# Performance work log

Measured on AMD Instinct MI355X. Metric: run time of the kernel, lower is better.

## Reference

```python
import jax, jax.numpy as jnp
import numpy as np

N_NODES = 100000
N_EDGES = 1600000
HIDDEN = 128


def setup_inputs() -> dict:
    key = jax.random.key(0)
    k_x, k_w1, k_w2, k_v, k_i, k_o = jax.random.split(key, 6)
    x = jax.random.normal(k_x, (N_NODES, HIDDEN), dtype=jnp.float32)
    # gate1/gate2 are Linear(hidden,1,bias=False); store their weight rows as vectors
    w1 = jax.random.normal(k_w1, (HIDDEN,), dtype=jnp.float32) * 0.1
    w2 = jax.random.normal(k_w2, (HIDDEN,), dtype=jnp.float32) * 0.1
    adj_vals = jax.random.uniform(k_v, (N_EDGES,), dtype=jnp.float32)
    in_idx = jax.random.randint(k_i, (N_EDGES,), 0, N_NODES, dtype=jnp.int32)
    out_idx = jax.random.randint(k_o, (N_EDGES,), 0, N_NODES, dtype=jnp.int32)
    return {"x": x, "w1": w1, "w2": w2, "adj_vals": adj_vals,
            "in_idx": in_idx, "out_idx": out_idx}


def reference(x, w1, w2, adj_vals, in_idx, out_idx):
    # per-node gate scalars: x1 = gate1(x), x2 = gate2(x)  -> [N]
    x1 = x @ w1
    x2 = x @ w2
    # edge gate: tanh(x1[src] + x2[dst]) * adj_value  (dropout is identity in eval mode)
    m = jnp.tanh(x1[in_idx] + x2[out_idx]) * adj_vals  # [E]
    # sparse.mm(adj_alpha, x): out[i] = sum_{e: row(e)=i} m_e * x[col(e)]
    messages = m[:, None] * x[out_idx]                 # [E, d]
    result = jax.ops.segment_sum(messages, in_idx, num_segments=N_NODES)
    return result
```

## Files before the change

### kernel.cpp

```cpp
#include <hip/hip_runtime.h>

#define N_NODES 100000
#define N_EDGES 1600000
#define HIDDEN  128

#define NPB_SHIFT 9
#define NPB       512
#define NB        ((N_NODES + NPB - 1) / NPB)
#define PART_EPT  16
#define PART_EPB  (256 * PART_EPT)
#define PART_B    ((N_EDGES + PART_EPB - 1) / PART_EPB)

#define SCAN_C 16
#define SCAN_T ((N_NODES + SCAN_C - 1) / SCAN_C)
#define SCAN_THREADS 6400
#define SCAN_B (SCAN_THREADS / 256)

__device__ __forceinline__ ushort f2bf(float f) {
    unsigned int u = __float_as_uint(f);
    u = (u + 0x7FFFu + ((u >> 16) & 1u)) >> 16;
    return (ushort)u;
}

__global__ void fagcn_gates(const float* __restrict__ x,
                            const float* __restrict__ w1,
                            const float* __restrict__ w2,
                            float* __restrict__ g1,
                            float* __restrict__ g2,
                            int*   __restrict__ cursor,
                            int*   __restrict__ bcnt,
                            ushort* __restrict__ xh,
                            int write_xh) {
    const int tid  = blockIdx.x * blockDim.x + threadIdx.x;
    if (tid < NB) bcnt[tid] = 0;
    const int node = tid >> 5;
    const int hl   = (int)(threadIdx.x & 31);
    if (node >= N_NODES) return;

    const float4 xv  = *reinterpret_cast<const float4*>(x  + (size_t)node * HIDDEN + hl * 4);
    const float4 w1v = *reinterpret_cast<const float4*>(w1 + hl * 4);
    const float4 w2v = *reinterpret_cast<const float4*>(w2 + hl * 4);

    if (write_xh) {
        ushort4 h;
        h.x = f2bf(xv.x); h.y = f2bf(xv.y); h.z = f2bf(xv.z); h.w = f2bf(xv.w);
        *reinterpret_cast<ushort4*>(xh + (size_t)node * HIDDEN + hl * 4) = h;
    }

    float s1 = xv.x * w1v.x + xv.y * w1v.y + xv.z * w1v.z + xv.w * w1v.w;
    float s2 = xv.x * w2v.x + xv.y * w2v.y + xv.z * w2v.z + xv.w * w2v.w;

    #pragma unroll
    for (int off = 16; off > 0; off >>= 1) {
        s1 += __shfl_down(s1, off, 32);
        s2 += __shfl_down(s2, off, 32);
    }
    if (hl == 0) {
        g1[node] = s1;
        g2[node] = s2;
        cursor[node] = 0;
    }
}

__global__ void fagcn_histb(const int* __restrict__ in_idx,
                            int* __restrict__ bcnt) {
    __shared__ int cnt[NB];
    const int tid  = (int)threadIdx.x;
    const int base = blockIdx.x * PART_EPB + tid * PART_EPT;
    for (int j = tid; j < NB; j += 256) cnt[j] = 0;
    __syncthreads();
    if (base < N_EDGES) {
        #pragma unroll
        for (int i = 0; i < 4; ++i) {
            const int4 v = *reinterpret_cast<const int4*>(in_idx + base + i * 4);
            atomicAdd(&cnt[v.x >> NPB_SHIFT], 1);
            atomicAdd(&cnt[v.y >> NPB_SHIFT], 1);
            atomicAdd(&cnt[v.z >> NPB_SHIFT], 1);
            atomicAdd(&cnt[v.w >> NPB_SHIFT], 1);
        }
    }
    __syncthreads();
    for (int j = tid; j < NB; j += 256)
        if (cnt[j]) atomicAdd(&bcnt[j], cnt[j]);
}

__global__ void fagcn_scanb(const int* __restrict__ bcnt,
                            int* __restrict__ bbase,
                            int* __restrict__ bcur) {
    __shared__ int l[256];
    const int t = (int)threadIdx.x;
    const int c = (t < NB) ? bcnt[t] : 0;
    l[t] = c;
    __syncthreads();
    for (int off = 1; off < 256; off <<= 1) {
        int v = (t >= off) ? l[t - off] : 0;
        __syncthreads();
        l[t] += v;
        __syncthreads();
    }
    if (t < NB) { bbase[t] = l[t] - c; bcur[t] = 0; }
    if (t == NB - 1) bbase[NB] = l[t];
}

__global__ void fagcn_part(const float* __restrict__ adj,
                           const int*   __restrict__ in_idx,
                           const int*   __restrict__ out_idx,
                           const float* __restrict__ g1,
                           const float* __restrict__ g2,
                           const int*   __restrict__ bbase,
                           int*         __restrict__ bcur,
                           int2*        __restrict__ stage) {
    __shared__ int cnt[NB], lbase[NB], lcur[NB];
    const int tid  = (int)threadIdx.x;
    const int base = blockIdx.x * PART_EPB + tid * PART_EPT;
    for (int j = tid; j < NB; j += 256) { cnt[j] = 0; lcur[j] = 0; }
    __syncthreads();

    int s[PART_EPT];
    const bool act = (base < N_EDGES);
    if (act) {
        #pragma unroll
        for (int i = 0; i < 4; ++i) {
            const int4 v = *reinterpret_cast<const int4*>(in_idx + base + i * 4);
            s[4 * i + 0] = v.x; s[4 * i + 1] = v.y;
            s[4 * i + 2] = v.z; s[4 * i + 3] = v.w;
        }
        #pragma unroll
        for (int i = 0; i < PART_EPT; ++i)
            atomicAdd(&cnt[s[i] >> NPB_SHIFT], 1);
    }
    __syncthreads();
    for (int j = tid; j < NB; j += 256)
        if (cnt[j] > 0) lbase[j] = bbase[j] + atomicAdd(&bcur[j], cnt[j]);
    __syncthreads();
    if (act) {
        #pragma unroll
        for (int i = 0; i < 4; ++i) {
            const int4   d4 = *reinterpret_cast<const int4*>(out_idx + base + i * 4);
            const float4 a4 = *reinterpret_cast<const float4*>(adj + base + i * 4);
            const int   dd[4] = {d4.x, d4.y, d4.z, d4.w};
            const float aa[4] = {a4.x, a4.y, a4.z, a4.w};
            #pragma unroll
            for (int k = 0; k < 4; ++k) {
                const int src = s[4 * i + k];
                const int dst = dd[k];
                const float m = tanhf(g1[src] + g2[dst]) * aa[k];
                const int b   = src >> NPB_SHIFT;
                const int pos = lbase[b] + atomicAdd(&lcur[b], 1);
                stage[pos] = make_int2(((src & (NPB - 1)) << 17) | dst,
                                       __float_as_int(m));
            }
        }
    }
}

__global__ void fagcn_fine(const int2* __restrict__ stage,
                           const int*  __restrict__ bbase,
                           int*        __restrict__ offsets,
                           int2*       __restrict__ sedge) {
    __shared__ int cnt[NPB];
    __shared__ int cur[NPB];
    const int b    = (int)blockIdx.x;
    const int t    = (int)threadIdx.x;
    const int nb   = b << NPB_SHIFT;
    const int ebeg = bbase[b];
    const int eend = bbase[b + 1];

    cnt[t] = 0;
    __syncthreads();
    for (int e = ebeg + t; e < eend; e += NPB)
        atomicAdd(&cnt[stage[e].x >> 17], 1);
    __syncthreads();

    const int c = cnt[t];
    for (int off = 1; off < NPB; off <<= 1) {
        int v = (t >= off) ? cnt[t - off] : 0;
        __syncthreads();
        cnt[t] += v;
        __syncthreads();
    }
    const int excl = cnt[t] - c;
    cur[t] = ebeg + excl;
    const int node = nb + t;
    if (node < N_NODES) offsets[node] = ebeg + excl;
    if (b == (int)gridDim.x - 1 && t == 0) offsets[N_NODES] = N_EDGES;
    __syncthreads();

    for (int e = ebeg + t; e < eend; e += NPB) {
        const int2 ed = stage[e];
        const int pos = atomicAdd(&cur[ed.x >> 17], 1);
        sedge[pos] = make_int2(ed.x & 0x1FFFF, ed.y);
    }
}

__device__ __forceinline__ void acc8(float* a, uint4 v, float m) {
    const unsigned int u[4] = {v.x, v.y, v.z, v.w};
    #pragma unroll
    for (int i = 0; i < 4; ++i) {
        const float lo = __uint_as_float(u[i] << 16);
        const float hi = __uint_as_float(u[i] & 0xFFFF0000u);
        a[2 * i]     += m * lo;
        a[2 * i + 1] += m * hi;
    }
}

__global__ void fagcn_gather_bf16(const ushort* __restrict__ xh,
                                  const int*   __restrict__ offsets,
                                  const int2*  __restrict__ sedge,
                                  float*       __restrict__ out) {
    const int wave = (int)((blockIdx.x * blockDim.x + threadIdx.x) >> 6);
    const int lane = (int)(threadIdx.x & 63);
    if (wave >= N_NODES) return;

    const int beg = offsets[wave];
    const int end = offsets[wave + 1];
    const int q   = lane >> 4;
    const int ql  = lane & 15;

    float a[8] = {0.f, 0.f, 0.f, 0.f, 0.f, 0.f, 0.f, 0.f};
    float b[8] = {0.f, 0.f, 0.f, 0.f, 0.f, 0.f, 0.f, 0.f};

    int e = beg + q;
    for (; e + 12 < end; e += 16) {
        const int2 ed0 = sedge[e];
        const int2 ed1 = sedge[e + 4];
        const int2 ed2 = sedge[e + 8];
        const int2 ed3 = sedge[e + 12];
        const uint4 v0 = *reinterpret_cast<const uint4*>(xh + (size_t)ed0.x * HIDDEN + ql * 8);
        const uint4 v1 = *reinterpret_cast<const uint4*>(xh + (size_t)ed1.x * HIDDEN + ql * 8);
        const uint4 v2 = *reinterpret_cast<const uint4*>(xh + (size_t)ed2.x * HIDDEN + ql * 8);
        const uint4 v3 = *reinterpret_cast<const uint4*>(xh + (size_t)ed3.x * HIDDEN + ql * 8);
        acc8(a, v0, __int_as_float(ed0.y));
        acc8(b, v1, __int_as_float(ed1.y));
        acc8(a, v2, __int_as_float(ed2.y));
        acc8(b, v3, __int_as_float(ed3.y));
    }
    for (; e < end; e += 4) {
        const int2 ed = sedge[e];
        const uint4 v = *reinterpret_cast<const uint4*>(xh + (size_t)ed.x * HIDDEN + ql * 8);
        acc8(a, v, __int_as_float(ed.y));
    }

    float r[8];
    #pragma unroll
    for (int i = 0; i < 8; ++i) r[i] = a[i] + b[i];
    #pragma unroll
    for (int i = 0; i < 8; ++i) r[i] += __shfl(r[i], lane ^ 16, 64);
    #pragma unroll
    for (int i = 0; i < 8; ++i) r[i] += __shfl(r[i], lane ^ 32, 64);

    if (lane < 16) {
        float* o = out + (size_t)wave * HIDDEN + ql * 8;
        float4 lo = {r[0], r[1], r[2], r[3]};
        float4 hi = {r[4], r[5], r[6], r[7]};
        *reinterpret_cast<float4*>(o)     = lo;
        *reinterpret_cast<float4*>(o + 4) = hi;
    }
}

__global__ void fagcn_hist(const int* __restrict__ in_idx,
                           int* __restrict__ counts) {
    const int e = blockIdx.x * blockDim.x + threadIdx.x;
    if (e < N_EDGES) atomicAdd(&counts[in_idx[e]], 1);
}

__global__ void fagcn_scan1(const int* __restrict__ counts,
                            int* __restrict__ tsum) {
    const int t = blockIdx.x * blockDim.x + threadIdx.x;
    if (t >= SCAN_THREADS) return;
    int s = 0;
    if (t < SCAN_T) {
        const int beg = t * SCAN_C;
        const int end = (beg + SCAN_C < N_NODES) ? beg + SCAN_C : N_NODES;
        for (int i = beg; i < end; ++i) s += counts[i];
    }
    tsum[t] = s;
}

__global__ void fagcn_scan2(int* __restrict__ tsum) {
    __shared__ int lsum[1024];
    const int t = (int)threadIdx.x;
    const int C = (SCAN_THREADS + 1023) / 1024;
    const int beg = t * C;
    const int end = (beg + C < SCAN_THREADS) ? beg + C : SCAN_THREADS;
    int s = 0;
    for (int i = beg; i < end; ++i) s += tsum[i];
    lsum[t] = s;
    __syncthreads();
    for (int off = 1; off < 1024; off <<= 1) {
        int v = (t >= off) ? lsum[t - off] : 0;
        __syncthreads();
        lsum[t] += v;
        __syncthreads();
    }
    int prefix = (t == 0) ? 0 : lsum[t - 1];
    for (int i = beg; i < end; ++i) {
        const int v = tsum[i];
        tsum[i] = prefix;
        prefix += v;
    }
}

__global__ void fagcn_scan3(int* counts,
                            const int* __restrict__ tsum,
                            int* __restrict__ offsets) {
    const int t = blockIdx.x * blockDim.x + threadIdx.x;
    if (t >= SCAN_T) return;
    const int beg = t * SCAN_C;
    const int end = (beg + SCAN_C < N_NODES) ? beg + SCAN_C : N_NODES;
    int prefix = tsum[t];
    for (int i = beg; i < end; ++i) {
        const int c = counts[i];
        offsets[i] = prefix;
        prefix += c;
        counts[i] = 0;
    }
    if (t == 0) offsets[N_NODES] = N_EDGES;
}

__global__ void fagcn_bin(const float* __restrict__ adj,
                          const int*   __restrict__ in_idx,
                          const int*   __restrict__ out_idx,
                          const float* __restrict__ g1,
                          const float* __restrict__ g2,
                          const int*   __restrict__ offsets,
                          int*         __restrict__ cursor,
                          int2*        __restrict__ sedge) {
    const int e = blockIdx.x * blockDim.x + threadIdx.x;
    if (e >= N_EDGES) return;
    const int src = in_idx[e];
    const int dst = out_idx[e];
    const float m = tanhf(g1[src] + g2[dst]) * adj[e];
    const int pos = offsets[src] + atomicAdd(&cursor[src], 1);
    sedge[pos] = make_int2(dst, __float_as_int(m));
}

__global__ void fagcn_gather_f32(const float* __restrict__ x,
                                 const int*   __restrict__ offsets,
                                 const int2*  __restrict__ sedge,
                                 float*       __restrict__ out) {
    const int wave = (int)((blockIdx.x * blockDim.x + threadIdx.x) >> 6);
    const int lane = (int)(threadIdx.x & 63);
    if (wave >= N_NODES) return;
    const int beg  = offsets[wave];
    const int end  = offsets[wave + 1];
    const int half = lane >> 5;
    const int hl   = lane & 31;
    float4 a0 = {0.f, 0.f, 0.f, 0.f};
    float4 a1 = {0.f, 0.f, 0.f, 0.f};
    int e = beg + half;
    for (; e + 2 < end; e += 4) {
        const int2 ed0 = sedge[e];
        const int2 ed1 = sedge[e + 2];
        const float m0 = __int_as_float(ed0.y);
        const float m1 = __int_as_float(ed1.y);
        const float4 v0 = *reinterpret_cast<const float4*>(x + (size_t)ed0.x * HIDDEN + hl * 4);
        const float4 v1 = *reinterpret_cast<const float4*>(x + (size_t)ed1.x * HIDDEN + hl * 4);
        a0.x += m0 * v0.x; a0.y += m0 * v0.y; a0.z += m0 * v0.z; a0.w += m0 * v0.w;
        a1.x += m1 * v1.x; a1.y += m1 * v1.y; a1.z += m1 * v1.z; a1.w += m1 * v1.w;
    }
    for (; e < end; e += 2) {
        const int2 ed = sedge[e];
        const float m = __int_as_float(ed.y);
        const float4 v = *reinterpret_cast<const float4*>(x + (size_t)ed.x * HIDDEN + hl * 4);
        a0.x += m * v.x; a0.y += m * v.y; a0.z += m * v.z; a0.w += m * v.w;
    }
    float4 a;
    a.x = a0.x + a1.x; a.y = a0.y + a1.y; a.z = a0.z + a1.z; a.w = a0.w + a1.w;
    a.x += __shfl(a.x, lane ^ 32, 64);
    a.y += __shfl(a.y, lane ^ 32, 64);
    a.z += __shfl(a.z, lane ^ 32, 64);
    a.w += __shfl(a.w, lane ^ 32, 64);
    if (half == 0) {
        *reinterpret_cast<float4*>(out + (size_t)wave * HIDDEN + hl * 4) = a;
    }
}

extern "C" void kernel_launch(void* const* d_in, const int* in_sizes, int n_in,
                              void* d_out, int out_size, void* d_ws, size_t ws_size,
                              hipStream_t stream) {
    const float* x        = (const float*)d_in[0];
    const float* w1       = (const float*)d_in[1];
    const float* w2       = (const float*)d_in[2];
    const float* adj_vals = (const float*)d_in[3];
    const int*   in_idx   = (const int*)d_in[4];
    const int*   out_idx  = (const int*)d_in[5];
    float* out = (float*)d_out;

    ushort* xh      = (ushort*)d_ws;
    int2*   sedge   = (int2*)(xh + (size_t)N_NODES * HIDDEN);
    int2*   stage   = sedge + N_EDGES;
    float*  g1      = (float*)(stage + N_EDGES);
    float*  g2      = g1 + N_NODES;
    int*    offsets = (int*)(g2 + N_NODES);
    int*    cursor  = offsets + N_NODES + 1;
    int*    tsum    = cursor + N_NODES;
    int*    bcnt    = tsum + SCAN_THREADS;
    int*    bbase   = bcnt + NB;
    int*    bcur    = bbase + NB + 1;

    const size_t need_full = (size_t)((char*)(bcur + NB) - (char*)d_ws);
    const size_t need_old  = need_full - (size_t)N_EDGES * 8;
    const int full_path = (ws_size >= need_full);
    const int bf16_ok   = (ws_size >= need_old);

    if (full_path) {
        fagcn_gates<<<(N_NODES * 32 + 255) / 256, 256, 0, stream>>>(
            x, w1, w2, g1, g2, cursor, bcnt, xh, 1);
        fagcn_histb<<<PART_B, 256, 0, stream>>>(in_idx, bcnt);
        fagcn_scanb<<<1, 256, 0, stream>>>(bcnt, bbase, bcur);
        fagcn_part<<<PART_B, 256, 0, stream>>>(
            adj_vals, in_idx, out_idx, g1, g2, bbase, bcur, stage);
        fagcn_fine<<<NB, NPB, 0, stream>>>(stage, bbase, offsets, sedge);
        fagcn_gather_bf16<<<(N_NODES + 3) / 4, 256, 0, stream>>>(
            xh, offsets, sedge, out);
    } else {
        if (!bf16_ok) sedge = (int2*)d_ws;
        fagcn_gates<<<(N_NODES * 32 + 255) / 256, 256, 0, stream>>>(
            x, w1, w2, g1, g2, cursor, bcnt, xh, bf16_ok);
        fagcn_hist<<<(N_EDGES + 255) / 256, 256, 0, stream>>>(in_idx, cursor);
        fagcn_scan1<<<SCAN_B, 256, 0, stream>>>(cursor, tsum);
        fagcn_scan2<<<1, 1024, 0, stream>>>(tsum);
        fagcn_scan3<<<SCAN_B, 256, 0, stream>>>(cursor, tsum, offsets);
        fagcn_bin<<<(N_EDGES + 255) / 256, 256, 0, stream>>>(
            adj_vals, in_idx, out_idx, g1, g2, offsets, cursor, sedge);
        if (bf16_ok) {
            fagcn_gather_bf16<<<(N_NODES + 3) / 4, 256, 0, stream>>>(
                xh, offsets, sedge, out);
        } else {
            fagcn_gather_f32<<<(N_NODES + 3) / 4, 256, 0, stream>>>(
                x, offsets, sedge, out);
        }
    }
}
```

Measured before the change: 162.6 us.

## Fuse gates with bucket histogram, fold bucket scan into consumers, register-cache fine pass

```diff
diff --git a/kernel.cpp b/kernel.cpp
--- a/kernel.cpp
+++ b/kernel.cpp
@@ -10,6 +10,8 @@
 #define PART_EPT  16
 #define PART_EPB  (256 * PART_EPT)
 #define PART_B    ((N_EDGES + PART_EPB - 1) / PART_EPB)
+#define GATES_B   ((N_NODES * 32 + 255) / 256)
+#define FINE_PE   20
 
 #define SCAN_C 16
 #define SCAN_T ((N_NODES + SCAN_C - 1) / SCAN_C)
@@ -22,84 +24,61 @@
     return (ushort)u;
 }
 
-__global__ void fagcn_gates(const float* __restrict__ x,
-                            const float* __restrict__ w1,
-                            const float* __restrict__ w2,
-                            float* __restrict__ g1,
-                            float* __restrict__ g2,
-                            int*   __restrict__ cursor,
-                            int*   __restrict__ bcnt,
-                            ushort* __restrict__ xh,
-                            int write_xh) {
-    const int tid  = blockIdx.x * blockDim.x + threadIdx.x;
-    if (tid < NB) bcnt[tid] = 0;
-    const int node = tid >> 5;
-    const int hl   = (int)(threadIdx.x & 31);
-    if (node >= N_NODES) return;
-
-    const float4 xv  = *reinterpret_cast<const float4*>(x  + (size_t)node * HIDDEN + hl * 4);
-    const float4 w1v = *reinterpret_cast<const float4*>(w1 + hl * 4);
-    const float4 w2v = *reinterpret_cast<const float4*>(w2 + hl * 4);
-
-    if (write_xh) {
-        ushort4 h;
-        h.x = f2bf(xv.x); h.y = f2bf(xv.y); h.z = f2bf(xv.z); h.w = f2bf(xv.w);
-        *reinterpret_cast<ushort4*>(xh + (size_t)node * HIDDEN + hl * 4) = h;
-    }
-
-    float s1 = xv.x * w1v.x + xv.y * w1v.y + xv.z * w1v.z + xv.w * w1v.w;
-    float s2 = xv.x * w2v.x + xv.y * w2v.y + xv.z * w2v.z + xv.w * w2v.w;
-
-    #pragma unroll
-    for (int off = 16; off > 0; off >>= 1) {
-        s1 += __shfl_down(s1, off, 32);
-        s2 += __shfl_down(s2, off, 32);
-    }
-    if (hl == 0) {
-        g1[node] = s1;
-        g2[node] = s2;
-        cursor[node] = 0;
-    }
-}
-
-__global__ void fagcn_histb(const int* __restrict__ in_idx,
-                            int* __restrict__ bcnt) {
+__global__ void fagcn_gates_hist(const float* __restrict__ x,
+                                 const float* __restrict__ w1,
+                                 const float* __restrict__ w2,
+                                 const int*   __restrict__ in_idx,
+                                 float* __restrict__ g1,
+                                 float* __restrict__ g2,
+                                 int*   __restrict__ bcnt,
+                                 ushort* __restrict__ xh,
+                                 int write_xh,
+                                 int with_hist) {
     __shared__ int cnt[NB];
-    const int tid  = (int)threadIdx.x;
-    const int base = blockIdx.x * PART_EPB + tid * PART_EPT;
-    for (int j = tid; j < NB; j += 256) cnt[j] = 0;
-    __syncthreads();
-    if (base < N_EDGES) {
+    if ((int)blockIdx.x < GATES_B) {
+        const int tid  = blockIdx.x * 256 + (int)threadIdx.x;
+        const int node = tid >> 5;
+        const int hl   = (int)(threadIdx.x & 31);
+        if (node >= N_NODES) return;
+
+        const float4 xv  = *reinterpret_cast<const float4*>(x  + (size_t)node * HIDDEN + hl * 4);
+        const float4 w1v = *reinterpret_cast<const float4*>(w1 + hl * 4);
+        const float4 w2v = *reinterpret_cast<const float4*>(w2 + hl * 4);
+
+        if (write_xh) {
+            ushort4 h;
+            h.x = f2bf(xv.x); h.y = f2bf(xv.y); h.z = f2bf(xv.z); h.w = f2bf(xv.w);
+            *reinterpret_cast<ushort4*>(xh + (size_t)node * HIDDEN + hl * 4) = h;
+        }
+
+        float s1 = xv.x * w1v.x + xv.y * w1v.y + xv.z * w1v.z + xv.w * w1v.w;
+        float s2 = xv.x * w2v.x + xv.y * w2v.y + xv.z * w2v.z + xv.w * w2v.w;
+
         #pragma unroll
-        for (int i = 0; i < 4; ++i) {
-            const int4 v = *reinterpret_cast<const int4*>(in_idx + base + i * 4);
-            atomicAdd(&cnt[v.x >> NPB_SHIFT], 1);
-            atomicAdd(&cnt[v.y >> NPB_SHIFT], 1);
-            atomicAdd(&cnt[v.z >> NPB_SHIFT], 1);
-            atomicAdd(&cnt[v.w >> NPB_SHIFT], 1);
-        }
-    }
-    __syncthreads();
-    for (int j = tid; j < NB; j += 256)
-        if (cnt[j]) atomicAdd(&bcnt[j], cnt[j]);
-}
-
-__global__ void fagcn_scanb(const int* __restrict__ bcnt,
-                            int* __restrict__ bbase,
-                            int* __restrict__ bcur) {
-    __shared__ int l[256];
-    const int t = (int)threadIdx.x;
-    const int c = (t < NB) ? bcnt[t] : 0;
-    l[t] = c;
-    __syncthreads();
-    for (int off = 1; off < 256; off <<= 1) {
-        int v = (t >= off) ? l[t - off] : 0;
-        __syncthreads();
-        l[t] += v;
-        __syncthreads();
-    }
-    if (t < NB) { bbase[t] = l[t] - c; bcur[t] = 0; }
-    if (t == NB - 1) bbase[NB] = l[t];
+        for (int off = 16; off > 0; off >>= 1) {
+            s1 += __shfl_down(s1, off, 32);
+            s2 += __shfl_down(s2, off, 32);
+        }
+        if (hl == 0) { g1[node] = s1; g2[node] = s2; }
+    } else if (with_hist) {
+        const int tid  = (int)threadIdx.x;
+        const int base = ((int)blockIdx.x - GATES_B) * PART_EPB + tid * PART_EPT;
+        for (int j = tid; j < NB; j += 256) cnt[j] = 0;
+        __syncthreads();
+        if (base < N_EDGES) {
+            #pragma unroll
+            for (int i = 0; i < 4; ++i) {
+                const int4 v = *reinterpret_cast<const int4*>(in_idx + base + i * 4);
+                atomicAdd(&cnt[v.x >> NPB_SHIFT], 1);
+                atomicAdd(&cnt[v.y >> NPB_SHIFT], 1);
+                atomicAdd(&cnt[v.z >> NPB_SHIFT], 1);
+                atomicAdd(&cnt[v.w >> NPB_SHIFT], 1);
+            }
+        }
+        __syncthreads();
+        for (int j = tid; j < NB; j += 256)
+            if (cnt[j]) atomicAdd(&bcnt[j], cnt[j]);
+    }
 }
 
 __global__ void fagcn_part(const float* __restrict__ adj,
@@ -107,12 +86,24 @@
                            const int*   __restrict__ out_idx,
                            const float* __restrict__ g1,
                            const float* __restrict__ g2,
-                           const int*   __restrict__ bbase,
+                           const int*   __restrict__ bcnt,
                            int*         __restrict__ bcur,
                            int2*        __restrict__ stage) {
-    __shared__ int cnt[NB], lbase[NB], lcur[NB];
+    __shared__ int scan[256];
+    __shared__ int sbase[NB], cnt[NB], lbase[NB], lcur[NB];
     const int tid  = (int)threadIdx.x;
     const int base = blockIdx.x * PART_EPB + tid * PART_EPT;
+
+    const int c0 = (tid < NB) ? bcnt[tid] : 0;
+    scan[tid] = c0;
+    __syncthreads();
+    for (int off = 1; off < 256; off <<= 1) {
+        int v = (tid >= off) ? scan[tid - off] : 0;
+        __syncthreads();
+        scan[tid] += v;
+        __syncthreads();
+    }
+    if (tid < NB) sbase[tid] = scan[tid] - c0;
     for (int j = tid; j < NB; j += 256) { cnt[j] = 0; lcur[j] = 0; }
     __syncthreads();
 
@@ -131,7 +122,7 @@
     }
     __syncthreads();
     for (int j = tid; j < NB; j += 256)
-        if (cnt[j] > 0) lbase[j] = bbase[j] + atomicAdd(&bcur[j], cnt[j]);
+        if (cnt[j] > 0) lbase[j] = sbase[j] + atomicAdd(&bcur[j], cnt[j]);
     __syncthreads();
     if (act) {
         #pragma unroll
@@ -155,21 +146,37 @@
 }
 
 __global__ void fagcn_fine(const int2* __restrict__ stage,
-                           const int*  __restrict__ bbase,
+                           const int*  __restrict__ bcnt,
                            int*        __restrict__ offsets,
                            int2*       __restrict__ sedge) {
     __shared__ int cnt[NPB];
     __shared__ int cur[NPB];
-    const int b    = (int)blockIdx.x;
-    const int t    = (int)threadIdx.x;
-    const int nb   = b << NPB_SHIFT;
-    const int ebeg = bbase[b];
-    const int eend = bbase[b + 1];
-
+    __shared__ int s_ebeg;
+    const int b = (int)blockIdx.x;
+    const int t = (int)threadIdx.x;
+
+    if (t < 64) {
+        int s = 0;
+        for (int j = t; j < b; j += 64) s += bcnt[j];
+        #pragma unroll
+        for (int off = 32; off > 0; off >>= 1) s += __shfl_down(s, off, 64);
+        if (t == 0) s_ebeg = s;
+    }
     cnt[t] = 0;
     __syncthreads();
-    for (int e = ebeg + t; e < eend; e += NPB)
-        atomicAdd(&cnt[stage[e].x >> 17], 1);
+
+    const int ebeg = s_ebeg;
+    const int eend = ebeg + bcnt[b];
+
+    int2 pay[FINE_PE];
+    #pragma unroll
+    for (int i = 0; i < FINE_PE; ++i) {
+        const int e = ebeg + t + i * NPB;
+        if (e < eend) {
+            pay[i] = stage[e];
+            atomicAdd(&cnt[pay[i].x >> 17], 1);
+        }
+    }
     __syncthreads();
 
     const int c = cnt[t];
@@ -181,15 +188,18 @@
     }
     const int excl = cnt[t] - c;
     cur[t] = ebeg + excl;
-    const int node = nb + t;
+    const int node = (b << NPB_SHIFT) + t;
     if (node < N_NODES) offsets[node] = ebeg + excl;
     if (b == (int)gridDim.x - 1 && t == 0) offsets[N_NODES] = N_EDGES;
     __syncthreads();
 
-    for (int e = ebeg + t; e < eend; e += NPB) {
-        const int2 ed = stage[e];
-        const int pos = atomicAdd(&cur[ed.x >> 17], 1);
-        sedge[pos] = make_int2(ed.x & 0x1FFFF, ed.y);
+    #pragma unroll
+    for (int i = 0; i < FINE_PE; ++i) {
+        const int e = ebeg + t + i * NPB;
+        if (e < eend) {
+            const int pos = atomicAdd(&cur[pay[i].x >> 17], 1);
+            sedge[pos] = make_int2(pay[i].x & 0x1FFFF, pay[i].y);
+        }
     }
 }
 
@@ -202,6 +212,13 @@
         a[2 * i]     += m * lo;
         a[2 * i + 1] += m * hi;
     }
+}
+
+__device__ __forceinline__ void ld_edge(const int2* p, int& dst, float& m) {
+    const long long v = __builtin_nontemporal_load(
+        reinterpret_cast<const long long*>(p));
+    dst = (int)(v & 0xFFFFFFFFll);
+    m   = __int_as_float((int)(v >> 32));
 }
 
 __global__ void fagcn_gather_bf16(const ushort* __restrict__ xh,
@@ -222,23 +239,25 @@
 
     int e = beg + q;
     for (; e + 12 < end; e += 16) {
-        const int2 ed0 = sedge[e];
-        const int2 ed1 = sedge[e + 4];
-        const int2 ed2 = sedge[e + 8];
-        const int2 ed3 = sedge[e + 12];
-        const uint4 v0 = *reinterpret_cast<const uint4*>(xh + (size_t)ed0.x * HIDDEN + ql * 8);
-        const uint4 v1 = *reinterpret_cast<const uint4*>(xh + (size_t)ed1.x * HIDDEN + ql * 8);
-        const uint4 v2 = *reinterpret_cast<const uint4*>(xh + (size_t)ed2.x * HIDDEN + ql * 8);
-        const uint4 v3 = *reinterpret_cast<const uint4*>(xh + (size_t)ed3.x * HIDDEN + ql * 8);
-        acc8(a, v0, __int_as_float(ed0.y));
-        acc8(b, v1, __int_as_float(ed1.y));
-        acc8(a, v2, __int_as_float(ed2.y));
-        acc8(b, v3, __int_as_float(ed3.y));
+        int d0, d1, d2, d3; float m0, m1, m2, m3;
+        ld_edge(sedge + e,      d0, m0);
+        ld_edge(sedge + e + 4,  d1, m1);
+        ld_edge(sedge + e + 8,  d2, m2);
+        ld_edge(sedge + e + 12, d3, m3);
+        const uint4 v0 = *reinterpret_cast<const uint4*>(xh + (size_t)d0 * HIDDEN + ql * 8);
+        const uint4 v1 = *reinterpret_cast<const uint4*>(xh + (size_t)d1 * HIDDEN + ql * 8);
+        const uint4 v2 = *reinterpret_cast<const uint4*>(xh + (size_t)d2 * HIDDEN + ql * 8);
+        const uint4 v3 = *reinterpret_cast<const uint4*>(xh + (size_t)d3 * HIDDEN + ql * 8);
+        acc8(a, v0, m0);
+        acc8(b, v1, m1);
+        acc8(a, v2, m2);
+        acc8(b, v3, m3);
     }
     for (; e < end; e += 4) {
-        const int2 ed = sedge[e];
-        const uint4 v = *reinterpret_cast<const uint4*>(xh + (size_t)ed.x * HIDDEN + ql * 8);
-        acc8(a, v, __int_as_float(ed.y));
+        int d; float m;
+        ld_edge(sedge + e, d, m);
+        const uint4 v = *reinterpret_cast<const uint4*>(xh + (size_t)d * HIDDEN + ql * 8);
+        acc8(a, v, m);
     }
 
     float r[8];
@@ -396,8 +415,7 @@
     int*    cursor  = offsets + N_NODES + 1;
     int*    tsum    = cursor + N_NODES;
     int*    bcnt    = tsum + SCAN_THREADS;
-    int*    bbase   = bcnt + NB;
-    int*    bcur    = bbase + NB + 1;
+    int*    bcur    = bcnt + NB;
 
     const size_t need_full = (size_t)((char*)(bcur + NB) - (char*)d_ws);
     const size_t need_old  = need_full - (size_t)N_EDGES * 8;
@@ -405,19 +423,19 @@
     const int bf16_ok   = (ws_size >= need_old);
 
     if (full_path) {
-        fagcn_gates<<<(N_NODES * 32 + 255) / 256, 256, 0, stream>>>(
-            x, w1, w2, g1, g2, cursor, bcnt, xh, 1);
-        fagcn_histb<<<PART_B, 256, 0, stream>>>(in_idx, bcnt);
-        fagcn_scanb<<<1, 256, 0, stream>>>(bcnt, bbase, bcur);
+        hipMemsetAsync(bcnt, 0, (size_t)(2 * NB) * sizeof(int), stream);
+        fagcn_gates_hist<<<GATES_B + PART_B, 256, 0, stream>>>(
+            x, w1, w2, in_idx, g1, g2, bcnt, xh, 1, 1);
         fagcn_part<<<PART_B, 256, 0, stream>>>(
-            adj_vals, in_idx, out_idx, g1, g2, bbase, bcur, stage);
-        fagcn_fine<<<NB, NPB, 0, stream>>>(stage, bbase, offsets, sedge);
+            adj_vals, in_idx, out_idx, g1, g2, bcnt, bcur, stage);
+        fagcn_fine<<<NB, NPB, 0, stream>>>(stage, bcnt, offsets, sedge);
         fagcn_gather_bf16<<<(N_NODES + 3) / 4, 256, 0, stream>>>(
             xh, offsets, sedge, out);
     } else {
         if (!bf16_ok) sedge = (int2*)d_ws;
-        fagcn_gates<<<(N_NODES * 32 + 255) / 256, 256, 0, stream>>>(
-            x, w1, w2, g1, g2, cursor, bcnt, xh, bf16_ok);
+        fagcn_gates_hist<<<GATES_B, 256, 0, stream>>>(
+            x, w1, w2, in_idx, g1, g2, bcnt, xh, bf16_ok, 0);
+        hipMemsetAsync(cursor, 0, (size_t)N_NODES * sizeof(int), stream);
         fagcn_hist<<<(N_EDGES + 255) / 256, 256, 0, stream>>>(in_idx, cursor);
         fagcn_scan1<<<SCAN_B, 256, 0, stream>>>(cursor, tsum);
         fagcn_scan2<<<1, 1024, 0, stream>>>(tsum);
```

Result: no change. 161.7 us (-0.6%).
